# Kernel tuning notes

Hardware: AMD Instinct MI355X
Metric: run time of the kernel (lower is better)

Reference implementation:

```python
import jax, jax.numpy as jnp
import numpy as np

B, V, H, L = 256, 50000, 1024, 2

def setup_inputs() -> dict:
    key = jax.random.key(0)
    ks = jax.random.split(key, 9)
    s = 1.0 / np.sqrt(H)
    return {
        "input_ids": jax.random.randint(ks[0], (B,), 0, V),
        "hidden": jax.random.normal(ks[1], (L, B, H), jnp.float32),
        "emb": jax.random.normal(ks[2], (V, H), jnp.float32) * 0.02,
        "w_ih": jax.random.uniform(ks[3], (L, 3 * H, H), jnp.float32, -s, s),
        "w_hh": jax.random.uniform(ks[4], (L, 3 * H, H), jnp.float32, -s, s),
        "b_ih": jax.random.uniform(ks[5], (L, 3 * H), jnp.float32, -s, s),
        "b_hh": jax.random.uniform(ks[6], (L, 3 * H), jnp.float32, -s, s),
        "dec_w": jax.random.uniform(ks[7], (V, H), jnp.float32, -s, s),
        "dec_b": jax.random.uniform(ks[8], (V,), jnp.float32, -s, s),
    }

def _gru_cell(x, h, w_ih_l, w_hh_l, b_ih_l, b_hh_l):
    # PyTorch GRU cell math. x: [B,H], h: [B,H]
    gi = x @ w_ih_l.T + b_ih_l          # [B, 3H]
    gh = h @ w_hh_l.T + b_hh_l          # [B, 3H]
    i_r, i_z, i_n = jnp.split(gi, 3, axis=-1)
    h_r, h_z, h_n = jnp.split(gh, 3, axis=-1)
    r = jax.nn.sigmoid(i_r + h_r)
    z = jax.nn.sigmoid(i_z + h_z)
    n = jnp.tanh(i_n + r * h_n)
    return (1.0 - z) * n + z * h

def reference(input_ids, hidden, emb, w_ih, w_hh, b_ih, b_hh, dec_w, dec_b):
    x = emb[input_ids]                  # embedding gather: [B, H]
    new_h = []
    for l in range(hidden.shape[0]):    # small fixed n_layers loop
        h_new = _gru_cell(x, hidden[l], w_ih[l], w_hh[l], b_ih[l], b_hh[l])
        new_h.append(h_new)
        x = h_new                       # output of layer l feeds layer l+1
    hidden_out = jnp.stack(new_h)       # [L, B, H]
    logits = x @ dec_w.T + dec_b        # [B, V]
    return logits, hidden_out
```

## Files before the change

kernel.cpp:

```cpp
#include <hip/hip_runtime.h>

#define KDIM 1024

typedef __attribute__((ext_vector_type(8))) short bf16x8;
typedef __attribute__((ext_vector_type(4))) short short4v;
typedef __attribute__((ext_vector_type(4))) float f32x4;

__device__ __forceinline__ short f2bf(float f) {
    union { float f; unsigned u; } x; x.f = f;
    unsigned r = x.u + 0x7fffu + ((x.u >> 16) & 1u);
    return (short)(r >> 16);
}

__device__ __forceinline__ bf16x8 cvt8(f32x4 a, f32x4 b) {
    union { unsigned u[4]; bf16x8 v; } r;
    asm("v_cvt_pk_bf16_f32 %0, %1, %2" : "=v"(r.u[0]) : "v"(a.x), "v"(a.y));
    asm("v_cvt_pk_bf16_f32 %0, %1, %2" : "=v"(r.u[1]) : "v"(a.z), "v"(a.w));
    asm("v_cvt_pk_bf16_f32 %0, %1, %2" : "=v"(r.u[2]) : "v"(b.x), "v"(b.y));
    asm("v_cvt_pk_bf16_f32 %0, %1, %2" : "=v"(r.u[3]) : "v"(b.z), "v"(b.w));
    return r.v;
}

__device__ __forceinline__ void gload16(const void* g, void* l) {
    __builtin_amdgcn_global_load_lds(
        (const __attribute__((address_space(1))) void*)g,
        (__attribute__((address_space(3))) void*)l, 16, 0, 0);
}

#define WAIT_VM(n) asm volatile("s_waitcnt vmcnt(" #n ")" ::: "memory")
#define BARRIER() do { asm volatile("" ::: "memory"); \
                       __builtin_amdgcn_s_barrier();  \
                       asm volatile("" ::: "memory"); } while (0)

__launch_bounds__(512, 1)
__global__ void gemm_dec(const short* __restrict__ A, const float* __restrict__ W,
                         float* __restrict__ C, const float* __restrict__ bias, int N)
{
    constexpr int BUFB = 49152;
    __shared__ __align__(1024) char lds[3 * BUFB];

    const int n0 = blockIdx.x * 256;
    const int t = threadIdx.x;
    const int lane = t & 63;
    const int w = t >> 6;
    const int wr = w >> 2;
    const int wc = w & 3;

    const short* gA[2];
    #pragma unroll
    for (int i = 0; i < 2; ++i)
        gA[i] = A + (size_t)(w * 2 + i) * 16384 + lane * 8;
    const float* gW[4];
    int wdst[4];
    #pragma unroll
    for (int i = 0; i < 4; ++i) {
        int q = w * 4 + i;
        int kc = q >> 3, hf = (q >> 2) & 1, j = q & 3;
        int colg = n0 + j * 64 + lane;
        colg = (colg < N) ? colg : (N - 1);
        gW[i] = W + (size_t)colg * KDIM + kc * 8 + hf * 4;
        wdst[i] = 16384 + kc * 8192 + hf * 4096 + j * 1024;
    }

    f32x4 acc[8][4];
    #pragma unroll
    for (int i = 0; i < 8; ++i)
        #pragma unroll
        for (int j = 0; j < 4; ++j)
            acc[i][j] = (f32x4){0.f, 0.f, 0.f, 0.f};

    auto stage = [&](int s, int buf) {
        char* base = lds + buf * BUFB;
        #pragma unroll
        for (int i = 0; i < 4; ++i)
            gload16(gW[i] + s * 32, base + wdst[i]);
        #pragma unroll
        for (int i = 0; i < 2; ++i)
            gload16(gA[i] + s * 512, base + (w * 2 + i) * 1024);
    };

    const int kc = lane >> 4;
    const int cl = lane & 15;

    auto compute = [&](int buf) {
        const char* base = lds + buf * BUFB;
        const char* Wb = base + 16384;
        bf16x8 bfr[4];
        #pragma unroll
        for (int nf = 0; nf < 4; ++nf) {
            const char* p = Wb + kc * 8192 + (wc * 64 + nf * 16 + cl) * 16;
            f32x4 lo = *(const f32x4*)(p);
            f32x4 hi = *(const f32x4*)(p + 4096);
            bfr[nf] = cvt8(lo, hi);
        }
        #pragma unroll
        for (int mf = 0; mf < 8; ++mf) {
            bf16x8 a = *(const bf16x8*)(base + (wr * 8 + mf) * 1024 + lane * 16);
            #pragma unroll
            for (int nf = 0; nf < 4; ++nf)
                acc[mf][nf] = __builtin_amdgcn_mfma_f32_16x16x32_bf16(a, bfr[nf], acc[mf][nf], 0, 0, 0);
        }
    };

    stage(0, 0);
    stage(1, 1);

    int bc = 0, bp = 2;
    for (int s = 0; s < 32; ++s) {
        if (s + 2 < 32) {
            stage(s + 2, bp);
            WAIT_VM(12);
        } else if (s + 2 == 32) {
            WAIT_VM(6);
        } else {
            WAIT_VM(0);
        }
        BARRIER();
        compute(bc);
        BARRIER();
        bc = (bc == 2) ? 0 : bc + 1;
        bp = (bp == 2) ? 0 : bp + 1;
    }

    #pragma unroll
    for (int mf = 0; mf < 8; ++mf) {
        int row = wr * 128 + mf * 16 + ((lane >> 4) << 2);
        #pragma unroll
        for (int nf = 0; nf < 4; ++nf) {
            int col = n0 + wc * 64 + nf * 16 + cl;
            if (col >= N) continue;
            float bv = bias[col];
            #pragma unroll
            for (int r = 0; r < 4; ++r)
                C[(size_t)(row + r) * N + col] = acc[mf][nf][r] + bv;
        }
    }
}

template<int NF, bool PRED>
__launch_bounds__(256, 2)
__global__ void gemm_pipe(const short* __restrict__ A0, const float* __restrict__ W0,
                          float* __restrict__ C0, int nb0,
                          const short* __restrict__ A1, const float* __restrict__ W1,
                          float* __restrict__ C1,
                          const float* __restrict__ bias, int N, int ldc)
{
    constexpr int WBYTES = NF * 4096;
    constexpr int BUFB   = 16384 + WBYTES;
    __shared__ __align__(1024) char lds[3 * BUFB];

    const int bx = blockIdx.x;
    const short* A; const float* W; float* C; int n0;
    if (bx < nb0) { A = A0; W = W0; C = C0; n0 = bx * (32 * NF); }
    else          { A = A1; W = W1; C = C1; n0 = (bx - nb0) * (32 * NF); }

    const int t = threadIdx.x;
    const int lane = t & 63;
    const int w = t >> 6;
    const int wr = w >> 1;
    const int wc = w & 1;

    const float* gW[NF];
    #pragma unroll
    for (int i = 0; i < NF; ++i) {
        int sl = (i * 4 + w) * 64 + lane;
        int row = sl >> 3, cc = sl & 7;
        int rowg = n0 + row;
        if (PRED) rowg = (rowg < N) ? rowg : (N - 1);
        gW[i] = W + (size_t)rowg * KDIM + ((cc ^ (row & 7)) << 2);
    }
    const short* gA[4];
    #pragma unroll
    for (int j = 0; j < 4; ++j)
        gA[j] = A + (size_t)(j * 4 + w) * 16384 + lane * 8;

    f32x4 acc[8][NF];
    #pragma unroll
    for (int i = 0; i < 8; ++i)
        #pragma unroll
        for (int j = 0; j < NF; ++j)
            acc[i][j] = (f32x4){0.f, 0.f, 0.f, 0.f};

    auto stage = [&](int s, int buf) {
        char* base = lds + buf * BUFB;
        #pragma unroll
        for (int i = 0; i < NF; ++i)
            gload16(gW[i] + s * 32, base + 16384 + (i * 4 + w) * 1024);
        #pragma unroll
        for (int j = 0; j < 4; ++j)
            gload16(gA[j] + s * 512, base + (j * 4 + w) * 1024);
    };

    auto compute = [&](int buf) {
        const char* base = lds + buf * BUFB;
        const char* Wb = base + 16384;
        bf16x8 bfr[NF];
        #pragma unroll
        for (int nf = 0; nf < NF; ++nf) {
            int row = (wc * NF + nf) * 16 + (lane & 15);
            int c0 = (lane >> 4) << 1;
            f32x4 lo = *(const f32x4*)(Wb + row * 128 + ((c0 ^ (row & 7)) << 4));
            f32x4 hi = *(const f32x4*)(Wb + row * 128 + (((c0 + 1) ^ (row & 7)) << 4));
            bfr[nf] = cvt8(lo, hi);
        }
        #pragma unroll
        for (int mf = 0; mf < 8; ++mf) {
            bf16x8 a = *(const bf16x8*)(base + (wr * 8 + mf) * 1024 + lane * 16);
            #pragma unroll
            for (int nf = 0; nf < NF; ++nf)
                acc[mf][nf] = __builtin_amdgcn_mfma_f32_16x16x32_bf16(a, bfr[nf], acc[mf][nf], 0, 0, 0);
        }
    };

    stage(0, 0);
    stage(1, 1);

    int bc = 0, bp = 2;
    for (int s = 0; s < 32; ++s) {
        if (s + 2 < 32) {
            stage(s + 2, bp);
            if constexpr (NF == 2) WAIT_VM(12); else WAIT_VM(10);
        } else if (s + 2 == 32) {
            if constexpr (NF == 2) WAIT_VM(6); else WAIT_VM(5);
        } else {
            WAIT_VM(0);
        }
        BARRIER();
        compute(bc);
        BARRIER();
        bc = (bc == 2) ? 0 : bc + 1;
        bp = (bp == 2) ? 0 : bp + 1;
    }

    #pragma unroll
    for (int mf = 0; mf < 8; ++mf) {
        int row = wr * 128 + mf * 16 + ((lane >> 4) << 2);
        #pragma unroll
        for (int nf = 0; nf < NF; ++nf) {
            int col = n0 + (wc * NF + nf) * 16 + (lane & 15);
            if (PRED && col >= N) continue;
            float bv = bias ? bias[col] : 0.0f;
            #pragma unroll
            for (int r = 0; r < 4; ++r)
                C[(size_t)(row + r) * ldc + col] = acc[mf][nf][r] + bv;
        }
    }
}

__global__ void prep_kernel(const int* __restrict__ ids, const float* __restrict__ hidden,
                            const float* __restrict__ emb,
                            short* __restrict__ x_frag, short* __restrict__ h_frag)
{
    const int m = blockIdx.x;
    const int which = blockIdx.y;
    const int j = threadIdx.x << 3;

    const float* src;
    short* dst;
    if (which == 0) { src = emb + (size_t)ids[m] * KDIM; dst = x_frag; }
    else {
        src = hidden + ((size_t)(which - 1) * 256 + m) * KDIM;
        dst = h_frag + (size_t)(which - 1) * 256 * KDIM;
    }
    f32x4 v0 = *(const f32x4*)(src + j);
    f32x4 v1 = *(const f32x4*)(src + j + 4);
    int mf = m >> 4, rr = m & 15, kf = j >> 5, g = (j >> 3) & 3;
    short* p = dst + (size_t)((mf * 32 + kf) * 64 + g * 16 + rr) * 8;
    short4v a, b;
    a.x = f2bf(v0.x); a.y = f2bf(v0.y); a.z = f2bf(v0.z); a.w = f2bf(v0.w);
    b.x = f2bf(v1.x); b.y = f2bf(v1.y); b.z = f2bf(v1.z); b.w = f2bf(v1.w);
    *(short4v*)p = a;
    *(short4v*)(p + 4) = b;
}

__global__ void gate_kernel(const float* __restrict__ gi, const float* __restrict__ gh,
                            const float* __restrict__ bi, const float* __restrict__ bh,
                            const float* __restrict__ hprev, float* __restrict__ hout,
                            short* __restrict__ x_frag)
{
    const int m = blockIdx.x;
    const int j = threadIdx.x << 3;
    const float* gim = gi + (size_t)m * 3072;
    const float* ghm = gh + (size_t)m * 3072;
    const float* hp = hprev + (size_t)m * KDIM;
    float* ho = hout + (size_t)m * KDIM;
    int mf = m >> 4, rr = m & 15, kf = j >> 5, g = (j >> 3) & 3;
    short* xp = x_frag + (size_t)((mf * 32 + kf) * 64 + g * 16 + rr) * 8;

    #pragma unroll
    for (int half = 0; half < 2; ++half) {
        int jj = j + half * 4;
        f32x4 vir = *(const f32x4*)(gim + jj);
        f32x4 viz = *(const f32x4*)(gim + 1024 + jj);
        f32x4 vin = *(const f32x4*)(gim + 2048 + jj);
        f32x4 vhr = *(const f32x4*)(ghm + jj);
        f32x4 vhz = *(const f32x4*)(ghm + 1024 + jj);
        f32x4 vhn = *(const f32x4*)(ghm + 2048 + jj);
        f32x4 bir = *(const f32x4*)(bi + jj);
        f32x4 biz = *(const f32x4*)(bi + 1024 + jj);
        f32x4 bin = *(const f32x4*)(bi + 2048 + jj);
        f32x4 bhr = *(const f32x4*)(bh + jj);
        f32x4 bhz = *(const f32x4*)(bh + 1024 + jj);
        f32x4 bhn = *(const f32x4*)(bh + 2048 + jj);
        f32x4 vh  = *(const f32x4*)(hp + jj);
        f32x4 outv;
        short4v xb;
        #pragma unroll
        for (int e = 0; e < 4; ++e) {
            float r = 1.f / (1.f + __expf(-(vir[e] + bir[e] + vhr[e] + bhr[e])));
            float z = 1.f / (1.f + __expf(-(viz[e] + biz[e] + vhz[e] + bhz[e])));
            float n = tanhf(vin[e] + bin[e] + r * (vhn[e] + bhn[e]));
            outv[e] = (1.f - z) * n + z * vh[e];
        }
        *(f32x4*)(ho + jj) = outv;
        xb.x = f2bf(outv[0]); xb.y = f2bf(outv[1]); xb.z = f2bf(outv[2]); xb.w = f2bf(outv[3]);
        *(short4v*)(xp + half * 4) = xb;
    }
}

extern "C" void kernel_launch(void* const* d_in, const int* in_sizes, int n_in,
                              void* d_out, int out_size, void* d_ws, size_t ws_size,
                              hipStream_t stream)
{
    const int*   ids    = (const int*)d_in[0];
    const float* hidden = (const float*)d_in[1];
    const float* emb    = (const float*)d_in[2];
    const float* w_ih   = (const float*)d_in[3];
    const float* w_hh   = (const float*)d_in[4];
    const float* b_ih   = (const float*)d_in[5];
    const float* b_hh   = (const float*)d_in[6];
    const float* dec_w  = (const float*)d_in[7];
    const float* dec_b  = (const float*)d_in[8];

    float* out = (float*)d_out;
    float* logits = out;
    float* hidden_out = out + (size_t)256 * 50000;

    short* x_frag = (short*)d_ws;
    short* h_frag = x_frag + 256 * 1024;
    float* gi = logits;
    float* gh = logits + (size_t)256 * 3072;

    prep_kernel<<<dim3(256, 3), 128, 0, stream>>>(ids, hidden, emb, x_frag, h_frag);

    for (int l = 0; l < 2; ++l) {
        gemm_pipe<1, false><<<192, 256, 0, stream>>>(
            x_frag, w_ih + (size_t)l * 3072 * 1024, gi, 96,
            h_frag + (size_t)l * 256 * 1024, w_hh + (size_t)l * 3072 * 1024, gh,
            nullptr, 3072, 3072);
        gate_kernel<<<256, 128, 0, stream>>>(
            gi, gh, b_ih + (size_t)l * 3072, b_hh + (size_t)l * 3072,
            hidden + (size_t)l * 256 * 1024,
            hidden_out + (size_t)l * 256 * 1024, x_frag);
    }

    gemm_dec<<<196, 512, 0, stream>>>(x_frag, dec_w, logits, dec_b, 50000);
}
```

Baseline: 124.8 us.

## Pre-transcode decoder weights to bf16 fragment layout before decoder GEMM

Adds a kernel that converts the fp32 decoder weight matrix into bf16, laid out in MFMA fragment order, in a workspace buffer on every call. The decoder GEMM then loads ready-made bf16 fragments directly, with no in-loop fp32-to-bf16 conversion and half the LDS staging per step. The trade is an extra full pass over the weights: an fp32 read plus a bf16 write before the GEMM, in place of the fused conversion.

```diff
diff --git a/kernel.cpp b/kernel.cpp
--- a/kernel.cpp
+++ b/kernel.cpp
@@ -27,39 +27,49 @@
         (__attribute__((address_space(3))) void*)l, 16, 0, 0);
 }
 
-#define WAIT_VM(n) asm volatile("s_waitcnt vmcnt(" #n ")" ::: "memory")
+#define WAIT_VM(n)  asm volatile("s_waitcnt vmcnt(" #n ")" ::: "memory")
 #define BARRIER() do { asm volatile("" ::: "memory"); \
                        __builtin_amdgcn_s_barrier();  \
                        asm volatile("" ::: "memory"); } while (0)
 
+__global__ void transcode_w(const float* __restrict__ W, short* __restrict__ out)
+{
+    const int gid = blockIdx.x * 256 + threadIdx.x;
+    const int n = gid >> 5, kf = gid & 31;
+    const float* src = W + (size_t)n * KDIM + kf * 32;
+    const int p = n >> 8, nr = n & 255, nf16 = nr >> 4, r = nr & 15;
+    short* dst = out + (size_t)p * 262144 + ((size_t)(nf16 * 32 + kf) * 64 + r) * 8;
+    #pragma unroll
+    for (int kc = 0; kc < 4; ++kc) {
+        f32x4 a = *(const f32x4*)(src + kc * 8);
+        f32x4 b = *(const f32x4*)(src + kc * 8 + 4);
+        *(bf16x8*)(dst + kc * 128) = cvt8(a, b);
+    }
+}
+
 __launch_bounds__(512, 1)
-__global__ void gemm_dec(const short* __restrict__ A, const float* __restrict__ W,
-                         float* __restrict__ C, const float* __restrict__ bias, int N)
-{
-    constexpr int BUFB = 49152;
-    __shared__ __align__(1024) char lds[3 * BUFB];
-
-    const int n0 = blockIdx.x * 256;
+__global__ void gemm_dec6(const short* __restrict__ A, const short* __restrict__ Wb,
+                          float* __restrict__ C, const float* __restrict__ bias, int N)
+{
+    __shared__ __align__(1024) char lds[3][32768];
+
+    const int p = blockIdx.x;
+    const int n0 = p * 256;
+    const short* Wp = Wb + (size_t)p * 262144;
+
     const int t = threadIdx.x;
     const int lane = t & 63;
     const int w = t >> 6;
     const int wr = w >> 2;
     const int wc = w & 3;
+    const int cl = lane & 15;
 
     const short* gA[2];
-    #pragma unroll
-    for (int i = 0; i < 2; ++i)
+    const short* gW[2];
+    #pragma unroll
+    for (int i = 0; i < 2; ++i) {
         gA[i] = A + (size_t)(w * 2 + i) * 16384 + lane * 8;
-    const float* gW[4];
-    int wdst[4];
-    #pragma unroll
-    for (int i = 0; i < 4; ++i) {
-        int q = w * 4 + i;
-        int kc = q >> 3, hf = (q >> 2) & 1, j = q & 3;
-        int colg = n0 + j * 64 + lane;
-        colg = (colg < N) ? colg : (N - 1);
-        gW[i] = W + (size_t)colg * KDIM + kc * 8 + hf * 4;
-        wdst[i] = 16384 + kc * 8192 + hf * 4096 + j * 1024;
+        gW[i] = Wp + (size_t)(w * 2 + i) * 16384 + lane * 8;
     }
 
     f32x4 acc[8][4];
@@ -70,29 +80,21 @@
             acc[i][j] = (f32x4){0.f, 0.f, 0.f, 0.f};
 
     auto stage = [&](int s, int buf) {
-        char* base = lds + buf * BUFB;
-        #pragma unroll
-        for (int i = 0; i < 4; ++i)
-            gload16(gW[i] + s * 32, base + wdst[i]);
+        char* base = lds[buf];
+        #pragma unroll
+        for (int i = 0; i < 2; ++i)
+            gload16(gW[i] + s * 512, base + 16384 + (w * 2 + i) * 1024);
         #pragma unroll
         for (int i = 0; i < 2; ++i)
             gload16(gA[i] + s * 512, base + (w * 2 + i) * 1024);
     };
 
-    const int kc = lane >> 4;
-    const int cl = lane & 15;
-
     auto compute = [&](int buf) {
-        const char* base = lds + buf * BUFB;
-        const char* Wb = base + 16384;
+        const char* base = lds[buf];
         bf16x8 bfr[4];
         #pragma unroll
-        for (int nf = 0; nf < 4; ++nf) {
-            const char* p = Wb + kc * 8192 + (wc * 64 + nf * 16 + cl) * 16;
-            f32x4 lo = *(const f32x4*)(p);
-            f32x4 hi = *(const f32x4*)(p + 4096);
-            bfr[nf] = cvt8(lo, hi);
-        }
+        for (int nf = 0; nf < 4; ++nf)
+            bfr[nf] = *(const bf16x8*)(base + 16384 + ((wc * 4 + nf) * 64 + lane) * 16);
         #pragma unroll
         for (int mf = 0; mf < 8; ++mf) {
             bf16x8 a = *(const bf16x8*)(base + (wr * 8 + mf) * 1024 + lane * 16);
@@ -109,9 +111,9 @@
     for (int s = 0; s < 32; ++s) {
         if (s + 2 < 32) {
             stage(s + 2, bp);
-            WAIT_VM(12);
+            WAIT_VM(8);
         } else if (s + 2 == 32) {
-            WAIT_VM(6);
+            WAIT_VM(4);
         } else {
             WAIT_VM(0);
         }
@@ -193,14 +195,14 @@
 
     auto compute = [&](int buf) {
         const char* base = lds + buf * BUFB;
-        const char* Wb = base + 16384;
+        const char* Wbp = base + 16384;
         bf16x8 bfr[NF];
         #pragma unroll
         for (int nf = 0; nf < NF; ++nf) {
             int row = (wc * NF + nf) * 16 + (lane & 15);
             int c0 = (lane >> 4) << 1;
-            f32x4 lo = *(const f32x4*)(Wb + row * 128 + ((c0 ^ (row & 7)) << 4));
-            f32x4 hi = *(const f32x4*)(Wb + row * 128 + (((c0 + 1) ^ (row & 7)) << 4));
+            f32x4 lo = *(const f32x4*)(Wbp + row * 128 + ((c0 ^ (row & 7)) << 4));
+            f32x4 hi = *(const f32x4*)(Wbp + row * 128 + (((c0 + 1) ^ (row & 7)) << 4));
             bfr[nf] = cvt8(lo, hi);
         }
         #pragma unroll
@@ -239,10 +241,10 @@
         for (int nf = 0; nf < NF; ++nf) {
             int col = n0 + (wc * NF + nf) * 16 + (lane & 15);
             if (PRED && col >= N) continue;
-            float bv = bias ? bias[col] : 0.0f;
+            float bvv = bias ? bias[col] : 0.0f;
             #pragma unroll
             for (int r = 0; r < 4; ++r)
-                C[(size_t)(row + r) * ldc + col] = acc[mf][nf][r] + bv;
+                C[(size_t)(row + r) * ldc + col] = acc[mf][nf][r] + bvv;
         }
     }
 }
@@ -265,12 +267,12 @@
     f32x4 v0 = *(const f32x4*)(src + j);
     f32x4 v1 = *(const f32x4*)(src + j + 4);
     int mf = m >> 4, rr = m & 15, kf = j >> 5, g = (j >> 3) & 3;
-    short* p = dst + (size_t)((mf * 32 + kf) * 64 + g * 16 + rr) * 8;
+    short* pp = dst + (size_t)((mf * 32 + kf) * 64 + g * 16 + rr) * 8;
     short4v a, b;
     a.x = f2bf(v0.x); a.y = f2bf(v0.y); a.z = f2bf(v0.z); a.w = f2bf(v0.w);
     b.x = f2bf(v1.x); b.y = f2bf(v1.y); b.z = f2bf(v1.z); b.w = f2bf(v1.w);
-    *(short4v*)p = a;
-    *(short4v*)(p + 4) = b;
+    *(short4v*)pp = a;
+    *(short4v*)(pp + 4) = b;
 }
 
 __global__ void gate_kernel(const float* __restrict__ gi, const float* __restrict__ gh,
@@ -338,10 +340,13 @@
 
     short* x_frag = (short*)d_ws;
     short* h_frag = x_frag + 256 * 1024;
+    short* w_bf   = (short*)((char*)d_ws + (size_t)16 * 1024 * 1024);
     float* gi = logits;
     float* gh = logits + (size_t)256 * 3072;
 
     prep_kernel<<<dim3(256, 3), 128, 0, stream>>>(ids, hidden, emb, x_frag, h_frag);
+
+    transcode_w<<<6250, 256, 0, stream>>>(dec_w, w_bf);
 
     for (int l = 0; l < 2; ++l) {
         gemm_pipe<1, false><<<192, 256, 0, stream>>>(
@@ -354,5 +359,5 @@
             hidden_out + (size_t)l * 256 * 1024, x_frag);
     }
 
-    gemm_dec<<<196, 512, 0, stream>>>(x_frag, dec_w, logits, dec_b, 50000);
-}
+    gemm_dec6<<<196, 512, 0, stream>>>(x_frag, w_bf, logits, dec_b, 50000);
+}
```

New measurement: 158.7 us. 27.1% more time.
